# Optimization experiments

Measured on AMD Instinct MI355X. Metric: run time of the kernel, lower is better.

Reference implementation:

```python
import jax, jax.numpy as jnp
import numpy as np

NEG = -9e15

def setup_inputs() -> dict:
    key = jax.random.key(0)
    k1, k2, k3, k4 = jax.random.split(key, 4)
    N, F_IN, F_OUT = 8192, 256, 256
    h = jax.random.normal(k1, (N, F_IN), dtype=jnp.float32)
    adj = jax.random.randint(k2, (N, N), 0, 2, dtype=jnp.int32)
    W = jax.random.normal(k3, (F_IN, F_OUT), dtype=jnp.float32) * (1.0 / np.sqrt(F_IN))
    a = jax.random.normal(k4, (2 * F_OUT,), dtype=jnp.float32) * (1.0 / np.sqrt(2 * F_OUT))
    return {"h": h, "adj": adj, "W": W, "a": a}

def reference(h, adj, W, a):
    # Wh: [N, F_out]
    Wh = h @ W
    F_OUT = Wh.shape[1]
    a1, a2 = a[:F_OUT], a[F_OUT:]
    # cat-based score decomposes: e_ij = leaky_relu(a1.Wh_i + a2.Wh_j)
    s1 = Wh @ a1  # [N]
    s2 = Wh @ a2  # [N]
    e = jax.nn.leaky_relu(s1[:, None] + s2[None, :], negative_slope=0.2)  # [N, N]
    e = jnp.where(adj > 0, e, NEG)
    attention = jax.nn.softmax(e, axis=-1)
    # dropout is identity in eval mode
    return attention @ Wh
```

## Files before the change

kernel.cpp:

```cpp
#include <hip/hip_runtime.h>

typedef short s8v  __attribute__((ext_vector_type(8)));
typedef float f4v  __attribute__((ext_vector_type(4)));
typedef int   v4i  __attribute__((ext_vector_type(4)));
typedef float v4f  __attribute__((ext_vector_type(4)));
typedef int   v2i  __attribute__((ext_vector_type(2)));

#define NNODES 8192
#define FDIM   256
#define NJC    4
#define JLEN   2048
#define TROWS  64
#define KSTEP  32
#define NSTEP  64

__device__ __forceinline__ float bf2f(unsigned short u) {
    unsigned int x = ((unsigned int)u) << 16;
    return __builtin_bit_cast(float, x);
}
__device__ __forceinline__ unsigned short f2bf(float f) {
    unsigned int x = __builtin_bit_cast(unsigned int, f);
    x += 0x7fffu + ((x >> 16) & 1u);
    return (unsigned short)(x >> 16);
}
__device__ __forceinline__ int cvt_pk(float lo, float hi) {
    int r;
    asm("v_cvt_pk_bf16_f32 %0, %1, %2" : "=v"(r) : "v"(lo), "v"(hi));
    return r;
}

__device__ __forceinline__ void barrier_lds_only() {
    asm volatile("s_waitcnt lgkmcnt(0)" ::: "memory");
    __builtin_amdgcn_s_barrier();
    asm volatile("" ::: "memory");
}

__global__ __launch_bounds__(256) void prep_kernel(const float* __restrict__ W,
                                                   const float* __restrict__ a,
                                                   unsigned short* __restrict__ WT,
                                                   float* __restrict__ v1,
                                                   float* __restrict__ v2) {
    if (blockIdx.x < 256) {
        int idx = blockIdx.x * 256 + threadIdx.x;
        int r = idx >> 8, c = idx & 255;
        WT[c * 256 + r] = f2bf(W[r * 256 + c]);
    } else {
        __shared__ float r1[256], r2[256];
        int b = blockIdx.x - 256, n = threadIdx.x;
        float w = W[(size_t)b * FDIM + n];
        r1[n] = w * a[n];
        r2[n] = w * a[FDIM + n];
        __syncthreads();
        for (int off = 128; off > 0; off >>= 1) {
            if (n < off) { r1[n] += r1[n + off]; r2[n] += r2[n + off]; }
            __syncthreads();
        }
        if (n == 0) { v1[b] = r1[0]; v2[b] = r2[0]; }
    }
}

__global__ __launch_bounds__(256) void wh_kernel(
    const float* __restrict__ h, const unsigned short* __restrict__ WT,
    const float* __restrict__ v1, const float* __restrict__ v2,
    unsigned short* __restrict__ PB,
    float* __restrict__ s1, float* __restrict__ s2)
{
    __shared__ float v1_lds[FDIM], v2_lds[FDIM];
    int tid = threadIdx.x;
    v1_lds[tid] = v1[tid];
    v2_lds[tid] = v2[tid];
    __syncthreads();

    int w = tid >> 6, lane = tid & 63, q = lane >> 4, l15 = lane & 15;
    int i_base = blockIdx.x * 64 + w * 16;

    f4v acc[16] = {};
    float s1p = 0.f, s2p = 0.f;

    for (int k0 = 0; k0 < 256; k0 += 32) {
        const float* hp = h + (size_t)(i_base + l15) * FDIM + k0 + q * 8;
        f4v h0 = *(const f4v*)hp;
        f4v h1 = *(const f4v*)(hp + 4);
        union { v4i u; s8v s; } af;
        af.u[0] = cvt_pk(h0[0], h0[1]);
        af.u[1] = cvt_pk(h0[2], h0[3]);
        af.u[2] = cvt_pk(h1[0], h1[1]);
        af.u[3] = cvt_pk(h1[2], h1[3]);
#pragma unroll
        for (int j = 0; j < 4; ++j) {
            s1p += h0[j] * v1_lds[k0 + q * 8 + j] + h1[j] * v1_lds[k0 + q * 8 + 4 + j];
            s2p += h0[j] * v2_lds[k0 + q * 8 + j] + h1[j] * v2_lds[k0 + q * 8 + 4 + j];
        }
#pragma unroll
        for (int t = 0; t < 16; ++t) {
            s8v bf = *(const s8v*)(WT + (size_t)(t * 16 + l15) * FDIM + k0 + q * 8);
            acc[t] = __builtin_amdgcn_mfma_f32_16x16x32_bf16(af.s, bf, acc[t], 0, 0, 0);
        }
    }

    s1p += __shfl_xor(s1p, 16, 64);
    s1p += __shfl_xor(s1p, 32, 64);
    s2p += __shfl_xor(s2p, 16, 64);
    s2p += __shfl_xor(s2p, 32, 64);
    if (lane < 16) {
        s1[i_base + lane] = s1p;
        s2[i_base + lane] = s2p;
    }

#pragma unroll
    for (int t = 0; t < 16; ++t) {
        int i0 = i_base + q * 4;
        size_t a16 = (size_t)((i0 >> 5) * 16 + t) * 512
                   + l15 * 32 + ((i0 >> 3) & 3) * 8 + (i0 & 7);
        v2i pk;
        pk[0] = cvt_pk(acc[t][0], acc[t][1]);
        pk[1] = cvt_pk(acc[t][2], acc[t][3]);
        *(v2i*)(PB + a16) = pk;
    }
}

__global__ __launch_bounds__(256, 3) void attn_partial(
    const int* __restrict__ adj, const unsigned short* __restrict__ PB,
    const float* __restrict__ s1, const float* __restrict__ s2,
    float* __restrict__ Npart, float* __restrict__ dpart)
{
    __shared__ float s2_lds[JLEN];
    __shared__ unsigned short P_lds[2][TROWS * KSTEP];
    __shared__ float dsum_lds[TROWS][4];

    int tid = threadIdx.x;
    int rt = blockIdx.x & 127, jc = blockIdx.x >> 7;
    int j0 = jc * JLEN;

    for (int i = tid; i < JLEN / 4; i += 256)
        ((v4f*)s2_lds)[i] = ((const v4f*)(s2 + j0))[i];

    int m = tid >> 2, idx = tid & 3;
    int row_g = rt * TROWS + m;
    float s1v = s1[row_g];
    const int* arow = adj + (size_t)row_g * NNODES + j0 + idx * 8;
    int woff = ((idx * 64 + m) * 8) ^ (idx * 16);

    int g = tid >> 6, lane = tid & 63, q = lane >> 4, l15 = lane & 15;
    const unsigned short* pbb = PB + (size_t)(jc * 64) * 16 * 512 + l15 * 32 + q * 8;

    f4v acc[4][4] = {};
    float dsum = 0.0f;

    __syncthreads();

    v4i a0 = __builtin_nontemporal_load((const v4i*)(arow));
    v4i a1 = __builtin_nontemporal_load((const v4i*)(arow + 4));
    v4i cur0 = __builtin_nontemporal_load((const v4i*)(arow + KSTEP));
    v4i cur1 = __builtin_nontemporal_load((const v4i*)(arow + KSTEP + 4));
    {
        int kb = idx * 8;
        v4f sA = *(const v4f*)&s2_lds[kb];
        v4f sB = *(const v4f*)&s2_lds[kb + 4];
        float pa[4], pb_[4];
#pragma unroll
        for (int j = 0; j < 4; ++j) {
            float x = s1v + sA[j];
            float p = (a0[j] > 0) ? __expf(fmaxf(x, 0.2f * x)) : 0.0f;
            pa[j] = p; dsum += p;
            float x2 = s1v + sB[j];
            float p2 = (a1[j] > 0) ? __expf(fmaxf(x2, 0.2f * x2)) : 0.0f;
            pb_[j] = p2; dsum += p2;
        }
        v4i pv;
        pv[0] = cvt_pk(pa[0], pa[1]);
        pv[1] = cvt_pk(pa[2], pa[3]);
        pv[2] = cvt_pk(pb_[0], pb_[1]);
        pv[3] = cvt_pk(pb_[2], pb_[3]);
        *(v4i*)&P_lds[0][woff] = pv;
    }
    barrier_lds_only();

    for (int s = 0; s < NSTEP; ++s) {
        int kn = (s < NSTEP - 2) ? (s + 2) * KSTEP : 0;
        v4i nx0 = __builtin_nontemporal_load((const v4i*)(arow + kn));
        v4i nx1 = __builtin_nontemporal_load((const v4i*)(arow + kn + 4));

        s8v bf[4];
#pragma unroll
        for (int t = 0; t < 4; ++t)
            bf[t] = *(const s8v*)(pbb + (size_t)(s * 16 + g * 4 + t) * 512);

        if (s < NSTEP - 1) {
            int kb = (s + 1) * KSTEP + idx * 8;
            v4f sA = *(const v4f*)&s2_lds[kb];
            v4f sB = *(const v4f*)&s2_lds[kb + 4];
            float pa[4], pb_[4];
#pragma unroll
            for (int j = 0; j < 4; ++j) {
                float x = s1v + sA[j];
                float p = (cur0[j] > 0) ? __expf(fmaxf(x, 0.2f * x)) : 0.0f;
                pa[j] = p; dsum += p;
                float x2 = s1v + sB[j];
                float p2 = (cur1[j] > 0) ? __expf(fmaxf(x2, 0.2f * x2)) : 0.0f;
                pb_[j] = p2; dsum += p2;
            }
            v4i pv;
            pv[0] = cvt_pk(pa[0], pa[1]);
            pv[1] = cvt_pk(pa[2], pa[3]);
            pv[2] = cvt_pk(pb_[0], pb_[1]);
            pv[3] = cvt_pk(pb_[2], pb_[3]);
            *(v4i*)&P_lds[(s + 1) & 1][woff] = pv;
        }

        const unsigned short* pbuf = P_lds[s & 1];
#pragma unroll
        for (int rh = 0; rh < 4; ++rh) {
            s8v af = *(const s8v*)&pbuf[((q * 64 + rh * 16 + l15) * 8) ^ (q * 16)];
#pragma unroll
            for (int t = 0; t < 4; ++t)
                acc[rh][t] = __builtin_amdgcn_mfma_f32_16x16x32_bf16(af, bf[t], acc[rh][t], 0, 0, 0);
        }

        barrier_lds_only();
        cur0 = nx0; cur1 = nx1;
    }

    dsum_lds[m][idx] = dsum;
    __syncthreads();
    if (tid < TROWS) {
        float d = dsum_lds[tid][0] + dsum_lds[tid][1] + dsum_lds[tid][2] + dsum_lds[tid][3];
        dpart[jc * NNODES + rt * TROWS + tid] = d;
    }

#pragma unroll
    for (int rh = 0; rh < 4; ++rh)
#pragma unroll
        for (int r = 0; r < 4; ++r) {
            int row = rh * 16 + q * 4 + r;
            float* base = Npart + ((size_t)(jc * NNODES) + rt * TROWS + row) * FDIM;
#pragma unroll
            for (int t = 0; t < 4; ++t)
                __builtin_nontemporal_store(acc[rh][t][r], base + g * 64 + t * 16 + l15);
        }
}

__global__ __launch_bounds__(256) void reduce_kernel(
    const float* __restrict__ Npart, const float* __restrict__ dpart,
    float* __restrict__ out)
{
    int i = blockIdx.x, n = threadIdx.x;
    float d = 0.f, acc = 0.f;
#pragma unroll
    for (int jc = 0; jc < NJC; ++jc) {
        d += dpart[jc * NNODES + i];
        acc += Npart[((size_t)(jc * NNODES) + i) * FDIM + n];
    }
    out[(size_t)i * FDIM + n] = acc / fmaxf(d, 1e-30f);
}

extern "C" void kernel_launch(void* const* d_in, const int* in_sizes, int n_in,
                              void* d_out, int out_size, void* d_ws, size_t ws_size,
                              hipStream_t stream) {
    const float* h   = (const float*)d_in[0];
    const int*   adj = (const int*)d_in[1];
    const float* W   = (const float*)d_in[2];
    const float* a   = (const float*)d_in[3];
    float* out = (float*)d_out;

    char* ws = (char*)d_ws;
    unsigned short* PB = (unsigned short*)ws;
    float* s1 = (float*)(ws + (4u << 20));
    float* s2 = (float*)(ws + (4u << 20) + (32u << 10));
    unsigned short* WT = (unsigned short*)(ws + (4u << 20) + (64u << 10));
    float* v1 = (float*)(ws + (4u << 20) + (192u << 10));
    float* v2 = (float*)(ws + (4u << 20) + (193u << 10));
    float* dpart = (float*)(ws + (5u << 20));
    float* Npart = (float*)(ws + (8u << 20));

    hipLaunchKernelGGL(prep_kernel, dim3(512), dim3(256), 0, stream, W, a, WT, v1, v2);
    hipLaunchKernelGGL(wh_kernel, dim3(128), dim3(256), 0, stream, h, WT, v1, v2, PB, s1, s2);
    hipLaunchKernelGGL(attn_partial, dim3(128 * NJC), dim3(256), 0, stream,
                       adj, PB, s1, s2, Npart, dpart);
    hipLaunchKernelGGL(reduce_kernel, dim3(NNODES), dim3(256), 0, stream, Npart, dpart, out);
}
```

Measured before the change: 439.0 us.

## Halve attention row tile to 32 and deepen adjacency prefetch to four steps

The attention row tile shrinks from 64 to 32 rows, so the partial kernel launches twice as many blocks with smaller accumulators, and occupancy is raised to 4 blocks per CU. Each thread now handles 4 adjacency columns instead of 8, with a three-deep register prefetch pipeline for the int32 adjacency stream. Block index mapping is changed so that the four j-chunks of one row tile are adjacent. wh_kernel is relaunched with 128 threads per block and 256 blocks. The cost is that each PB B-fragment loaded from global memory now feeds half as many MFMAs, which doubles PB read traffic per output.

```diff
diff --git a/kernel.cpp b/kernel.cpp
--- a/kernel.cpp
+++ b/kernel.cpp
@@ -10,7 +10,7 @@
 #define FDIM   256
 #define NJC    4
 #define JLEN   2048
-#define TROWS  64
+#define TROWS  32
 #define KSTEP  32
 #define NSTEP  64
 
@@ -59,7 +59,7 @@
     }
 }
 
-__global__ __launch_bounds__(256) void wh_kernel(
+__global__ __launch_bounds__(128) void wh_kernel(
     const float* __restrict__ h, const unsigned short* __restrict__ WT,
     const float* __restrict__ v1, const float* __restrict__ v2,
     unsigned short* __restrict__ PB,
@@ -67,12 +67,12 @@
 {
     __shared__ float v1_lds[FDIM], v2_lds[FDIM];
     int tid = threadIdx.x;
-    v1_lds[tid] = v1[tid];
-    v2_lds[tid] = v2[tid];
+    v1_lds[tid] = v1[tid];       v1_lds[tid + 128] = v1[tid + 128];
+    v2_lds[tid] = v2[tid];       v2_lds[tid + 128] = v2[tid + 128];
     __syncthreads();
 
     int w = tid >> 6, lane = tid & 63, q = lane >> 4, l15 = lane & 15;
-    int i_base = blockIdx.x * 64 + w * 16;
+    int i_base = blockIdx.x * 32 + w * 16;
 
     f4v acc[16] = {};
     float s1p = 0.f, s2p = 0.f;
@@ -119,67 +119,60 @@
     }
 }
 
-__global__ __launch_bounds__(256, 3) void attn_partial(
+__global__ __launch_bounds__(256, 4) void attn_partial(
     const int* __restrict__ adj, const unsigned short* __restrict__ PB,
     const float* __restrict__ s1, const float* __restrict__ s2,
     float* __restrict__ Npart, float* __restrict__ dpart)
 {
     __shared__ float s2_lds[JLEN];
     __shared__ unsigned short P_lds[2][TROWS * KSTEP];
-    __shared__ float dsum_lds[TROWS][4];
+    __shared__ float dsum_lds[TROWS][8];
 
     int tid = threadIdx.x;
-    int rt = blockIdx.x & 127, jc = blockIdx.x >> 7;
+    int jc = blockIdx.x & 3, rt = blockIdx.x >> 2;
     int j0 = jc * JLEN;
 
     for (int i = tid; i < JLEN / 4; i += 256)
         ((v4f*)s2_lds)[i] = ((const v4f*)(s2 + j0))[i];
 
-    int m = tid >> 2, idx = tid & 3;
+    int m = tid >> 3, idx = tid & 7;
     int row_g = rt * TROWS + m;
     float s1v = s1[row_g];
-    const int* arow = adj + (size_t)row_g * NNODES + j0 + idx * 8;
-    int woff = ((idx * 64 + m) * 8) ^ (idx * 16);
+    const int* arow = adj + (size_t)row_g * NNODES + j0 + idx * 4;
+    int q_w = idx >> 1, half = idx & 1;
+    int woff = (((q_w * 32 + m) * 8 + half * 4)) ^ (q_w * 16);
 
     int g = tid >> 6, lane = tid & 63, q = lane >> 4, l15 = lane & 15;
     const unsigned short* pbb = PB + (size_t)(jc * 64) * 16 * 512 + l15 * 32 + q * 8;
 
-    f4v acc[4][4] = {};
+    f4v acc[2][4] = {};
     float dsum = 0.0f;
 
     __syncthreads();
 
-    v4i a0 = __builtin_nontemporal_load((const v4i*)(arow));
-    v4i a1 = __builtin_nontemporal_load((const v4i*)(arow + 4));
-    v4i cur0 = __builtin_nontemporal_load((const v4i*)(arow + KSTEP));
-    v4i cur1 = __builtin_nontemporal_load((const v4i*)(arow + KSTEP + 4));
+    v4i p0 = __builtin_nontemporal_load((const v4i*)(arow));
+    v4i a1 = __builtin_nontemporal_load((const v4i*)(arow + 1 * KSTEP));
+    v4i a2 = __builtin_nontemporal_load((const v4i*)(arow + 2 * KSTEP));
+    v4i a3 = __builtin_nontemporal_load((const v4i*)(arow + 3 * KSTEP));
     {
-        int kb = idx * 8;
-        v4f sA = *(const v4f*)&s2_lds[kb];
-        v4f sB = *(const v4f*)&s2_lds[kb + 4];
-        float pa[4], pb_[4];
+        v4f sv = *(const v4f*)&s2_lds[idx * 4];
+        float pa[4];
 #pragma unroll
         for (int j = 0; j < 4; ++j) {
-            float x = s1v + sA[j];
-            float p = (a0[j] > 0) ? __expf(fmaxf(x, 0.2f * x)) : 0.0f;
+            float x = s1v + sv[j];
+            float p = (p0[j] > 0) ? __expf(fmaxf(x, 0.2f * x)) : 0.0f;
             pa[j] = p; dsum += p;
-            float x2 = s1v + sB[j];
-            float p2 = (a1[j] > 0) ? __expf(fmaxf(x2, 0.2f * x2)) : 0.0f;
-            pb_[j] = p2; dsum += p2;
-        }
-        v4i pv;
+        }
+        v2i pv;
         pv[0] = cvt_pk(pa[0], pa[1]);
         pv[1] = cvt_pk(pa[2], pa[3]);
-        pv[2] = cvt_pk(pb_[0], pb_[1]);
-        pv[3] = cvt_pk(pb_[2], pb_[3]);
-        *(v4i*)&P_lds[0][woff] = pv;
+        *(v2i*)&P_lds[0][woff] = pv;
     }
     barrier_lds_only();
 
     for (int s = 0; s < NSTEP; ++s) {
-        int kn = (s < NSTEP - 2) ? (s + 2) * KSTEP : 0;
-        v4i nx0 = __builtin_nontemporal_load((const v4i*)(arow + kn));
-        v4i nx1 = __builtin_nontemporal_load((const v4i*)(arow + kn + 4));
+        int kn = (s < NSTEP - 4) ? (s + 4) * KSTEP : 0;
+        v4i nx = __builtin_nontemporal_load((const v4i*)(arow + kn));
 
         s8v bf[4];
 #pragma unroll
@@ -187,49 +180,44 @@
             bf[t] = *(const s8v*)(pbb + (size_t)(s * 16 + g * 4 + t) * 512);
 
         if (s < NSTEP - 1) {
-            int kb = (s + 1) * KSTEP + idx * 8;
-            v4f sA = *(const v4f*)&s2_lds[kb];
-            v4f sB = *(const v4f*)&s2_lds[kb + 4];
-            float pa[4], pb_[4];
+            v4f sv = *(const v4f*)&s2_lds[(s + 1) * KSTEP + idx * 4];
+            float pa[4];
 #pragma unroll
             for (int j = 0; j < 4; ++j) {
-                float x = s1v + sA[j];
-                float p = (cur0[j] > 0) ? __expf(fmaxf(x, 0.2f * x)) : 0.0f;
+                float x = s1v + sv[j];
+                float p = (a1[j] > 0) ? __expf(fmaxf(x, 0.2f * x)) : 0.0f;
                 pa[j] = p; dsum += p;
-                float x2 = s1v + sB[j];
-                float p2 = (cur1[j] > 0) ? __expf(fmaxf(x2, 0.2f * x2)) : 0.0f;
-                pb_[j] = p2; dsum += p2;
             }
-            v4i pv;
+            v2i pv;
             pv[0] = cvt_pk(pa[0], pa[1]);
             pv[1] = cvt_pk(pa[2], pa[3]);
-            pv[2] = cvt_pk(pb_[0], pb_[1]);
-            pv[3] = cvt_pk(pb_[2], pb_[3]);
-            *(v4i*)&P_lds[(s + 1) & 1][woff] = pv;
+            *(v2i*)&P_lds[(s + 1) & 1][woff] = pv;
         }
 
         const unsigned short* pbuf = P_lds[s & 1];
 #pragma unroll
-        for (int rh = 0; rh < 4; ++rh) {
-            s8v af = *(const s8v*)&pbuf[((q * 64 + rh * 16 + l15) * 8) ^ (q * 16)];
+        for (int rh = 0; rh < 2; ++rh) {
+            s8v af = *(const s8v*)&pbuf[((q * 32 + rh * 16 + l15) * 8) ^ (q * 16)];
 #pragma unroll
             for (int t = 0; t < 4; ++t)
                 acc[rh][t] = __builtin_amdgcn_mfma_f32_16x16x32_bf16(af, bf[t], acc[rh][t], 0, 0, 0);
         }
 
         barrier_lds_only();
-        cur0 = nx0; cur1 = nx1;
+        a1 = a2; a2 = a3; a3 = nx;
     }
 
     dsum_lds[m][idx] = dsum;
     __syncthreads();
     if (tid < TROWS) {
-        float d = dsum_lds[tid][0] + dsum_lds[tid][1] + dsum_lds[tid][2] + dsum_lds[tid][3];
+        float d = 0.f;
+#pragma unroll
+        for (int k = 0; k < 8; ++k) d += dsum_lds[tid][k];
         dpart[jc * NNODES + rt * TROWS + tid] = d;
     }
 
 #pragma unroll
-    for (int rh = 0; rh < 4; ++rh)
+    for (int rh = 0; rh < 2; ++rh)
 #pragma unroll
         for (int r = 0; r < 4; ++r) {
             int row = rh * 16 + q * 4 + r;
@@ -274,8 +262,8 @@
     float* Npart = (float*)(ws + (8u << 20));
 
     hipLaunchKernelGGL(prep_kernel, dim3(512), dim3(256), 0, stream, W, a, WT, v1, v2);
-    hipLaunchKernelGGL(wh_kernel, dim3(128), dim3(256), 0, stream, h, WT, v1, v2, PB, s1, s2);
-    hipLaunchKernelGGL(attn_partial, dim3(128 * NJC), dim3(256), 0, stream,
+    hipLaunchKernelGGL(wh_kernel, dim3(256), dim3(128), 0, stream, h, WT, v1, v2, PB, s1, s2);
+    hipLaunchKernelGGL(attn_partial, dim3(256 * NJC), dim3(256), 0, stream,
                        adj, PB, s1, s2, Npart, dpart);
     hipLaunchKernelGGL(reduce_kernel, dim3(NNODES), dim3(256), 0, stream, Npart, dpart, out);
 }
```

Result: slower. 461.2 us (+5.1%).

## Warp-specialize attention kernel into producer and MFMA consumer wavefronts

Applied to the files above, without the earlier changes.

Splits attn_partial into 512-thread blocks where four wavefronts stream adj, compute exp scores and write bf16 P tiles to LDS, while four others prefetch Wh tiles and run MFMAs. The adj load queue deepens to four steps ahead, and the j-split drops from four chunks to two, which halves the partial-sum traffic for the reduce. wh_kernel is relaunched with smaller blocks to spread across more CUs. The change aims to overlap the adj memory stream with matrix math, at the cost of fewer blocks and more register pressure per block.

```diff
diff --git a/kernel.cpp b/kernel.cpp
--- a/kernel.cpp
+++ b/kernel.cpp
@@ -8,16 +8,12 @@
 
 #define NNODES 8192
 #define FDIM   256
-#define NJC    4
-#define JLEN   2048
+#define NJC    2
+#define JLEN   4096
 #define TROWS  64
 #define KSTEP  32
-#define NSTEP  64
-
-__device__ __forceinline__ float bf2f(unsigned short u) {
-    unsigned int x = ((unsigned int)u) << 16;
-    return __builtin_bit_cast(float, x);
-}
+#define NSTEP  128
+
 __device__ __forceinline__ unsigned short f2bf(float f) {
     unsigned int x = __builtin_bit_cast(unsigned int, f);
     x += 0x7fffu + ((x >> 16) & 1u);
@@ -59,7 +55,7 @@
     }
 }
 
-__global__ __launch_bounds__(256) void wh_kernel(
+__global__ __launch_bounds__(128) void wh_kernel(
     const float* __restrict__ h, const unsigned short* __restrict__ WT,
     const float* __restrict__ v1, const float* __restrict__ v2,
     unsigned short* __restrict__ PB,
@@ -67,12 +63,12 @@
 {
     __shared__ float v1_lds[FDIM], v2_lds[FDIM];
     int tid = threadIdx.x;
-    v1_lds[tid] = v1[tid];
-    v2_lds[tid] = v2[tid];
+    v1_lds[tid] = v1[tid];       v1_lds[tid + 128] = v1[tid + 128];
+    v2_lds[tid] = v2[tid];       v2_lds[tid + 128] = v2[tid + 128];
     __syncthreads();
 
     int w = tid >> 6, lane = tid & 63, q = lane >> 4, l15 = lane & 15;
-    int i_base = blockIdx.x * 64 + w * 16;
+    int i_base = blockIdx.x * 32 + w * 16;
 
     f4v acc[16] = {};
     float s1p = 0.f, s2p = 0.f;
@@ -119,7 +115,7 @@
     }
 }
 
-__global__ __launch_bounds__(256, 3) void attn_partial(
+__global__ __launch_bounds__(512, 2) void attn_partial(
     const int* __restrict__ adj, const unsigned short* __restrict__ PB,
     const float* __restrict__ s1, const float* __restrict__ s2,
     float* __restrict__ Npart, float* __restrict__ dpart)
@@ -129,43 +125,47 @@
     __shared__ float dsum_lds[TROWS][4];
 
     int tid = threadIdx.x;
-    int rt = blockIdx.x & 127, jc = blockIdx.x >> 7;
+    int jc = blockIdx.x & 1, rt = blockIdx.x >> 1;
     int j0 = jc * JLEN;
 
-    for (int i = tid; i < JLEN / 4; i += 256)
-        ((v4f*)s2_lds)[i] = ((const v4f*)(s2 + j0))[i];
-
-    int m = tid >> 2, idx = tid & 3;
-    int row_g = rt * TROWS + m;
-    float s1v = s1[row_g];
-    const int* arow = adj + (size_t)row_g * NNODES + j0 + idx * 8;
+    ((v4f*)s2_lds)[tid]       = ((const v4f*)(s2 + j0))[tid];
+    ((v4f*)s2_lds)[tid + 512] = ((const v4f*)(s2 + j0))[tid + 512];
+
+    bool producer = (tid >= 256);
+
+    int p = tid & 255, m = p >> 2, idx = p & 3;
     int woff = ((idx * 64 + m) * 8) ^ (idx * 16);
+    float s1v = 0.f;
+    const int* arow = adj + (size_t)(rt * TROWS + m) * NNODES + j0 + idx * 8;
+    v4i a1_0 = {}, a1_1 = {}, a2_0 = {}, a2_1 = {}, a3_0 = {}, a3_1 = {};
 
     int g = tid >> 6, lane = tid & 63, q = lane >> 4, l15 = lane & 15;
-    const unsigned short* pbb = PB + (size_t)(jc * 64) * 16 * 512 + l15 * 32 + q * 8;
-
+    const unsigned short* pbb = PB + (size_t)(jc * NSTEP) * 16 * 512 + l15 * 32 + q * 8;
     f4v acc[4][4] = {};
-    float dsum = 0.0f;
+    s8v bfA[4], bfB[4];
+    float dsum = 0.f;
 
     __syncthreads();
 
-    v4i a0 = __builtin_nontemporal_load((const v4i*)(arow));
-    v4i a1 = __builtin_nontemporal_load((const v4i*)(arow + 4));
-    v4i cur0 = __builtin_nontemporal_load((const v4i*)(arow + KSTEP));
-    v4i cur1 = __builtin_nontemporal_load((const v4i*)(arow + KSTEP + 4));
-    {
-        int kb = idx * 8;
-        v4f sA = *(const v4f*)&s2_lds[kb];
-        v4f sB = *(const v4f*)&s2_lds[kb + 4];
+    if (producer) {
+        s1v = s1[rt * TROWS + m];
+        v4i c0 = __builtin_nontemporal_load((const v4i*)(arow));
+        v4i c1 = __builtin_nontemporal_load((const v4i*)(arow + 4));
+        a1_0 = __builtin_nontemporal_load((const v4i*)(arow + 1 * KSTEP));
+        a1_1 = __builtin_nontemporal_load((const v4i*)(arow + 1 * KSTEP + 4));
+        a2_0 = __builtin_nontemporal_load((const v4i*)(arow + 2 * KSTEP));
+        a2_1 = __builtin_nontemporal_load((const v4i*)(arow + 2 * KSTEP + 4));
+        a3_0 = __builtin_nontemporal_load((const v4i*)(arow + 3 * KSTEP));
+        a3_1 = __builtin_nontemporal_load((const v4i*)(arow + 3 * KSTEP + 4));
+        v4f sA = *(const v4f*)&s2_lds[idx * 8];
+        v4f sB = *(const v4f*)&s2_lds[idx * 8 + 4];
         float pa[4], pb_[4];
 #pragma unroll
         for (int j = 0; j < 4; ++j) {
             float x = s1v + sA[j];
-            float p = (a0[j] > 0) ? __expf(fmaxf(x, 0.2f * x)) : 0.0f;
-            pa[j] = p; dsum += p;
+            pa[j] = (c0[j] > 0) ? __expf(fmaxf(x, 0.2f * x)) : 0.0f; dsum += pa[j];
             float x2 = s1v + sB[j];
-            float p2 = (a1[j] > 0) ? __expf(fmaxf(x2, 0.2f * x2)) : 0.0f;
-            pb_[j] = p2; dsum += p2;
+            pb_[j] = (c1[j] > 0) ? __expf(fmaxf(x2, 0.2f * x2)) : 0.0f; dsum += pb_[j];
         }
         v4i pv;
         pv[0] = cvt_pk(pa[0], pa[1]);
@@ -173,71 +173,83 @@
         pv[2] = cvt_pk(pb_[0], pb_[1]);
         pv[3] = cvt_pk(pb_[2], pb_[3]);
         *(v4i*)&P_lds[0][woff] = pv;
+    } else {
+#pragma unroll
+        for (int t = 0; t < 4; ++t)
+            bfA[t] = *(const s8v*)(pbb + (size_t)(g * 4 + t) * 512);
     }
     barrier_lds_only();
 
-    for (int s = 0; s < NSTEP; ++s) {
-        int kn = (s < NSTEP - 2) ? (s + 2) * KSTEP : 0;
-        v4i nx0 = __builtin_nontemporal_load((const v4i*)(arow + kn));
-        v4i nx1 = __builtin_nontemporal_load((const v4i*)(arow + kn + 4));
-
-        s8v bf[4];
-#pragma unroll
-        for (int t = 0; t < 4; ++t)
-            bf[t] = *(const s8v*)(pbb + (size_t)(s * 16 + g * 4 + t) * 512);
-
-        if (s < NSTEP - 1) {
-            int kb = (s + 1) * KSTEP + idx * 8;
-            v4f sA = *(const v4f*)&s2_lds[kb];
-            v4f sB = *(const v4f*)&s2_lds[kb + 4];
-            float pa[4], pb_[4];
-#pragma unroll
-            for (int j = 0; j < 4; ++j) {
-                float x = s1v + sA[j];
-                float p = (cur0[j] > 0) ? __expf(fmaxf(x, 0.2f * x)) : 0.0f;
-                pa[j] = p; dsum += p;
-                float x2 = s1v + sB[j];
-                float p2 = (cur1[j] > 0) ? __expf(fmaxf(x2, 0.2f * x2)) : 0.0f;
-                pb_[j] = p2; dsum += p2;
-            }
-            v4i pv;
-            pv[0] = cvt_pk(pa[0], pa[1]);
-            pv[1] = cvt_pk(pa[2], pa[3]);
-            pv[2] = cvt_pk(pb_[0], pb_[1]);
-            pv[3] = cvt_pk(pb_[2], pb_[3]);
-            *(v4i*)&P_lds[(s + 1) & 1][woff] = pv;
-        }
-
-        const unsigned short* pbuf = P_lds[s & 1];
-#pragma unroll
-        for (int rh = 0; rh < 4; ++rh) {
-            s8v af = *(const s8v*)&pbuf[((q * 64 + rh * 16 + l15) * 8) ^ (q * 16)];
-#pragma unroll
-            for (int t = 0; t < 4; ++t)
-                acc[rh][t] = __builtin_amdgcn_mfma_f32_16x16x32_bf16(af, bf[t], acc[rh][t], 0, 0, 0);
-        }
-
-        barrier_lds_only();
-        cur0 = nx0; cur1 = nx1;
-    }
-
-    dsum_lds[m][idx] = dsum;
+#define STEP(S, BCUR, BNXT) do {                                              \
+    if (!producer) {                                                          \
+        int sn = ((S) + 1 < NSTEP) ? (S) + 1 : 0;                             \
+        _Pragma("unroll")                                                     \
+        for (int t = 0; t < 4; ++t)                                           \
+            BNXT[t] = *(const s8v*)(pbb + (size_t)(sn * 16 + g * 4 + t) * 512);\
+        const unsigned short* pbuf = P_lds[(S) & 1];                          \
+        _Pragma("unroll")                                                     \
+        for (int rh = 0; rh < 4; ++rh) {                                      \
+            s8v af = *(const s8v*)&pbuf[((q * 64 + rh * 16 + l15) * 8) ^ (q * 16)]; \
+            _Pragma("unroll")                                                 \
+            for (int t = 0; t < 4; ++t)                                       \
+                acc[rh][t] = __builtin_amdgcn_mfma_f32_16x16x32_bf16(af, BCUR[t], acc[rh][t], 0, 0, 0); \
+        }                                                                     \
+    } else {                                                                  \
+        int kn = ((S) < NSTEP - 4) ? ((S) + 4) * KSTEP : 0;                   \
+        v4i nx0 = __builtin_nontemporal_load((const v4i*)(arow + kn));        \
+        v4i nx1 = __builtin_nontemporal_load((const v4i*)(arow + kn + 4));    \
+        if ((S) < NSTEP - 1) {                                                \
+            v4f sA = *(const v4f*)&s2_lds[((S) + 1) * KSTEP + idx * 8];       \
+            v4f sB = *(const v4f*)&s2_lds[((S) + 1) * KSTEP + idx * 8 + 4];   \
+            float pa[4], pb_[4];                                              \
+            _Pragma("unroll")                                                 \
+            for (int j = 0; j < 4; ++j) {                                     \
+                float x = s1v + sA[j];                                        \
+                pa[j] = (a1_0[j] > 0) ? __expf(fmaxf(x, 0.2f * x)) : 0.0f;    \
+                dsum += pa[j];                                                \
+                float x2 = s1v + sB[j];                                       \
+                pb_[j] = (a1_1[j] > 0) ? __expf(fmaxf(x2, 0.2f * x2)) : 0.0f; \
+                dsum += pb_[j];                                               \
+            }                                                                 \
+            v4i pv;                                                           \
+            pv[0] = cvt_pk(pa[0], pa[1]);                                     \
+            pv[1] = cvt_pk(pa[2], pa[3]);                                     \
+            pv[2] = cvt_pk(pb_[0], pb_[1]);                                   \
+            pv[3] = cvt_pk(pb_[2], pb_[3]);                                   \
+            *(v4i*)&P_lds[((S) + 1) & 1][woff] = pv;                          \
+        }                                                                     \
+        a1_0 = a2_0; a1_1 = a2_1;                                             \
+        a2_0 = a3_0; a2_1 = a3_1;                                             \
+        a3_0 = nx0;  a3_1 = nx1;                                              \
+    }                                                                         \
+    barrier_lds_only();                                                       \
+} while (0)
+
+    for (int sb = 0; sb < NSTEP; sb += 2) {
+        STEP(sb, bfA, bfB);
+        STEP(sb + 1, bfB, bfA);
+    }
+#undef STEP
+
+    if (producer) dsum_lds[m][idx] = dsum;
     __syncthreads();
     if (tid < TROWS) {
         float d = dsum_lds[tid][0] + dsum_lds[tid][1] + dsum_lds[tid][2] + dsum_lds[tid][3];
         dpart[jc * NNODES + rt * TROWS + tid] = d;
     }
 
-#pragma unroll
-    for (int rh = 0; rh < 4; ++rh)
-#pragma unroll
-        for (int r = 0; r < 4; ++r) {
-            int row = rh * 16 + q * 4 + r;
-            float* base = Npart + ((size_t)(jc * NNODES) + rt * TROWS + row) * FDIM;
-#pragma unroll
-            for (int t = 0; t < 4; ++t)
-                __builtin_nontemporal_store(acc[rh][t][r], base + g * 64 + t * 16 + l15);
-        }
+    if (!producer) {
+#pragma unroll
+        for (int rh = 0; rh < 4; ++rh)
+#pragma unroll
+            for (int r = 0; r < 4; ++r) {
+                int row = rh * 16 + q * 4 + r;
+                float* base = Npart + ((size_t)(jc * NNODES) + rt * TROWS + row) * FDIM;
+#pragma unroll
+                for (int t = 0; t < 4; ++t)
+                    __builtin_nontemporal_store(acc[rh][t][r], base + g * 64 + t * 16 + l15);
+            }
+    }
 }
 
 __global__ __launch_bounds__(256) void reduce_kernel(
@@ -274,8 +286,8 @@
     float* Npart = (float*)(ws + (8u << 20));
 
     hipLaunchKernelGGL(prep_kernel, dim3(512), dim3(256), 0, stream, W, a, WT, v1, v2);
-    hipLaunchKernelGGL(wh_kernel, dim3(128), dim3(256), 0, stream, h, WT, v1, v2, PB, s1, s2);
-    hipLaunchKernelGGL(attn_partial, dim3(128 * NJC), dim3(256), 0, stream,
+    hipLaunchKernelGGL(wh_kernel, dim3(256), dim3(128), 0, stream, h, WT, v1, v2, PB, s1, s2);
+    hipLaunchKernelGGL(attn_partial, dim3(128 * NJC), dim3(512), 0, stream,
                        adj, PB, s1, s2, Npart, dpart);
     hipLaunchKernelGGL(reduce_kernel, dim3(NNODES), dim3(256), 0, stream, Npart, dpart, out);
 }
```

New measurement: 462.0 us. 1.05x slower.
